# Performance work log

Measured on AMD Instinct MI355X. Metric: run time of the kernel, lower is better.

Reference implementation:

```python
import jax, jax.numpy as jnp
import numpy as np

N, H, W, PD, HID, NH = 2, 64, 64, 16, 128, 4
EPS = 1e-5


def _bn(x, g, b):
    # training-mode BatchNorm over (N, H, W) with biased variance, channels last
    m = jnp.mean(x, axis=(0, 1, 2), keepdims=True)
    v = jnp.var(x, axis=(0, 1, 2), keepdims=True)
    return (x - m) * jax.lax.rsqrt(v + EPS) * g + b


def _mha(x, in_w, in_b, out_w, out_b, nh):
    # torch nn.MultiheadAttention (batch_first) with packed qkv in_proj
    B, S, E = x.shape
    hd = E // nh
    q, k, v = jnp.split(x @ in_w.T + in_b, 3, axis=-1)
    def heads(t):
        return t.reshape(B, S, nh, hd).transpose(0, 2, 1, 3)  # B,nh,S,hd
    q, k, v = heads(q), heads(k), heads(v)
    a = jax.nn.softmax(jnp.einsum('bnqd,bnkd->bnqk', q, k) / np.float32(np.sqrt(hd)), axis=-1)
    o = jnp.einsum('bnqk,bnkd->bnqd', a, v).transpose(0, 2, 1, 3).reshape(B, S, E)
    return o @ out_w.T + out_b


def setup_inputs():
    key = jax.random.key(0)
    ks = jax.random.split(key, 32)
    def r(i, shape, s=0.1):
        return jax.random.normal(ks[i], shape, dtype=jnp.float32) * s
    mask = (jnp.arange(W) % 2) == 0  # alternating columns kept, M = W//2
    return {
        'kspace': jax.random.normal(ks[0], (N, 2, H, W), dtype=jnp.float32),
        'mask': mask,
        'pre_conv_w': r(1, (PD, 2), 0.5), 'pre_conv_b': r(2, (PD,)),
        'pre_pe_H': r(3, (H, PD)), 'pre_pe_W': r(4, (W, PD)),
        'res_conv1_w': r(5, (PD, PD), 0.2), 'res_conv1_b': r(6, (PD,)),
        'res_bn1_g': 1.0 + r(7, (PD,)), 'res_bn1_b': r(8, (PD,)),
        'res_conv2_w': r(9, (PD, PD), 0.2), 'res_conv2_b': r(10, (PD,)),
        'res_bn2_g': 1.0 + r(11, (PD,)), 'res_bn2_b': r(12, (PD,)),
        'proj_w': r(13, (HID, PD), 0.2), 'proj_b': r(14, (HID,)),
        'enc_in_w': r(15, (3 * HID, HID), 0.08), 'enc_in_b': r(16, (3 * HID,)),
        'enc_out_w': r(17, (HID, HID), 0.08), 'enc_out_b': r(18, (HID,)),
        'dec_pe_H': r(19, (H, HID)), 'dec_pe_W': r(20, (W, HID)),
        'dec_in_w': r(21, (3 * HID, HID), 0.08), 'dec_in_b': r(22, (3 * HID,)),
        'dec_out_w': r(23, (HID, HID), 0.08), 'dec_out_b': r(24, (HID,)),
        'masked_token': r(25, (HID,), 1.0),
        'post_w': r(26, (2, HID), 0.1), 'post_b': r(27, (2,)),
    }


def reference(kspace, mask, pre_conv_w, pre_conv_b, pre_pe_H, pre_pe_W,
              res_conv1_w, res_conv1_b, res_bn1_g, res_bn1_b,
              res_conv2_w, res_conv2_b, res_bn2_g, res_bn2_b,
              proj_w, proj_b, enc_in_w, enc_in_b, enc_out_w, enc_out_b,
              dec_pe_H, dec_pe_W, dec_in_w, dec_in_b, dec_out_w, dec_out_b,
              masked_token, post_w, post_b):
    cols = np.nonzero(np.asarray(mask))[0]  # static sampled columns
    M = cols.shape[0]
    # gather valid columns; channels last: [N, H, M, 2]
    x = kspace.transpose(0, 2, 3, 1)[:, :, cols, :]
    h = x @ pre_conv_w.T + pre_conv_b  # 1x1 conv -> [N, H, M, PD]
    h = h + (pre_pe_H[:, None, :] + pre_pe_W[cols][None, :, :])
    # PixelwiseConstantChannelResNet (1 layer)
    r1 = jax.nn.relu(_bn(h @ res_conv1_w.T + res_conv1_b, res_bn1_g, res_bn1_b))
    r2 = jax.nn.relu(_bn(r1 @ res_conv2_w.T + res_conv2_b, res_bn2_g, res_bn2_b))
    h = jax.nn.relu(h + r2)
    h = h @ proj_w.T + proj_b  # [N, H, M, HID]
    enc = _mha(h.reshape(N, H * M, HID), enc_in_w, enc_in_b, enc_out_w, enc_out_b, NH)
    # scatter: fill unmasked positions with masked_token, masked with encoder output
    dec = jnp.broadcast_to(masked_token, (N, H, W, HID))
    dec = dec.at[:, :, cols, :].set(enc.reshape(N, H, M, HID))
    dec = dec + (dec_pe_H[:, None, :] + dec_pe_W[None, :, :])
    dec = _mha(dec.reshape(N, H * W, HID), dec_in_w, dec_in_b, dec_out_w, dec_out_b, NH)
    out = dec.reshape(N, H, W, HID) @ post_w.T + post_b  # [N, H, W, 2]
    return out.transpose(0, 3, 1, 2)  # [N, 2, H, W]
```

## Files before the change

### kernel.cpp

```cpp
#include <hip/hip_runtime.h>
#include <math.h>

#define N_ 2
#define H_ 64
#define W_ 64
#define M_ 32
#define PD_ 16
#define HID_ 128
#define NH_ 4
#define HD_ 32
#define S_ENC 2048
#define S_DEC 4096
#define EPS_ 1e-5f
#define SCALE_ 0.17677669529663687f
#define SCALE2_ (0.17677669529663687f * 1.4426950408889634f)

#define OFF_H     0
#define OFF_T1    65536
#define OFF_T2    131072
#define OFF_STAT  196608
#define OFF_WP    196672
#define OFF_BP    202816
#define OFF_QBF   203264
#define OFF_KBF   727552
#define OFF_VTBF  1251840
#define OFF_ATTBF 1776128
#define OFF_XBF2  2300416
#define OFF_WBF   2824704

#define WOFF_ENC_OUT 0
#define WOFF_DEC_IN  16384
#define WOFF_DEC_OUT 65536

#define IB_MF   2048
#define IB_WC   320
#define IB_WP   24
#define IB_BP   2
#define IB_TOT  (IB_MF + IB_WC + IB_WP + IB_BP + 1)

typedef short bf16x8 __attribute__((ext_vector_type(8)));
typedef short bf16x4 __attribute__((ext_vector_type(4)));
typedef float f32x4 __attribute__((ext_vector_type(4)));

__device__ __forceinline__ short f2bf(float f) {
  union { float f; unsigned u; } v; v.f = f;
  unsigned r = v.u + 0x7FFFu + ((v.u >> 16) & 1u);
  return (short)(r >> 16);
}

__global__ void k_init(const float* __restrict__ eow, const float* __restrict__ dw,
                       const float* __restrict__ dow, const float* __restrict__ mt,
                       const float* __restrict__ peH, const float* __restrict__ peW,
                       const float* __restrict__ ew, const float* __restrict__ pw,
                       const float* __restrict__ pb, const float* __restrict__ eib,
                       short* __restrict__ wbf, short* __restrict__ xdec,
                       float* __restrict__ wp, float* __restrict__ bp,
                       float* __restrict__ stat) {
  int blk = blockIdx.x, tid = threadIdx.x;
  if (blk < IB_MF) {
    int idx = blk * 256 + tid;
    int j = idx & 127;
    int widx = (idx >> 7) & 31;
    int hh = (idx >> 12) & 63;
    int b = idx >> 18;
    int w = 2 * widx + 1;
    xdec[((size_t)(b * 4096 + hh * 64 + w)) * 128 + j] =
        f2bf(mt[j] + peH[hh * 128 + j] + peW[w * 128 + j]);
  } else if (blk < IB_MF + IB_WC) {
    int idx = (blk - IB_MF) * 256 + tid;
    float v;
    if (idx < 16384) v = eow[idx];
    else if (idx < 65536) v = dw[idx - 16384];
    else v = dow[idx - 65536];
    wbf[idx] = f2bf(v);
  } else if (blk < IB_MF + IB_WC + IB_WP) {
    int e = (blk - IB_MF - IB_WC) * 256 + tid;
    int row = e >> 4, k = e & 15;
    float a = 0.f;
    for (int j = 0; j < 128; j++) a = fmaf(ew[row * 128 + j], pw[j * 16 + k], a);
    wp[e] = a;
  } else if (blk < IB_MF + IB_WC + IB_WP + IB_BP) {
    int row = (blk - IB_MF - IB_WC - IB_WP) * 256 + tid;
    if (row < 384) {
      float a = eib[row];
      for (int j = 0; j < 128; j++) a = fmaf(ew[row * 128 + j], pb[j], a);
      bp[row] = a;
    }
  } else {
    if (tid < 64) stat[tid] = 0.f;
  }
}

__global__ void k_prelin_stats(const float* __restrict__ ks, const float* __restrict__ pcw,
                               const float* __restrict__ pcb, const float* __restrict__ peH,
                               const float* __restrict__ peW, const float* __restrict__ w1,
                               const float* __restrict__ b1, float* __restrict__ h,
                               float* __restrict__ t1, float* __restrict__ stat) {
  int tid = threadIdx.x;
  int pos = blockIdx.x * 256 + tid;
  int m = pos & 31, hh = (pos >> 5) & 63, b = pos >> 11;
  int w = 2 * m;
  float x0 = ks[((b * 2 + 0) * H_ + hh) * W_ + w];
  float x1 = ks[((b * 2 + 1) * H_ + hh) * W_ + w];
  float hv[16], tv[16];
#pragma unroll
  for (int c = 0; c < 16; c++)
    hv[c] = x0 * pcw[c * 2] + x1 * pcw[c * 2 + 1] + pcb[c]
            + peH[hh * PD_ + c] + peW[w * PD_ + c];
#pragma unroll
  for (int c = 0; c < 16; c += 4)
    *(float4*)&h[pos * 16 + c] = make_float4(hv[c], hv[c + 1], hv[c + 2], hv[c + 3]);
#pragma unroll
  for (int c = 0; c < 16; c++) {
    float a = b1[c];
#pragma unroll
    for (int k = 0; k < 16; k++) a = fmaf(hv[k], w1[c * 16 + k], a);
    tv[c] = a;
    t1[pos * 16 + c] = a;
  }
  __shared__ float tl[256][17];
#pragma unroll
  for (int c = 0; c < 16; c++) tl[tid][c] = tv[c];
  __syncthreads();
  int c = tid & 15, g = tid >> 4;
  float s = 0.f, s2 = 0.f;
#pragma unroll
  for (int r = 0; r < 16; r++) {
    float v = tl[g * 16 + r][c];
    s += v; s2 += v * v;
  }
  __shared__ float ps[16][16], ps2[16][16];
  ps[g][c] = s; ps2[g][c] = s2;
  __syncthreads();
  if (tid < 16) {
    float S = 0.f, S2 = 0.f;
#pragma unroll
    for (int g2 = 0; g2 < 16; g2++) { S += ps[g2][tid]; S2 += ps2[g2][tid]; }
    atomicAdd(&stat[tid], S);
    atomicAdd(&stat[16 + tid], S2);
  }
}

__global__ void k_bnlin_stats(const float* __restrict__ t1, const float* __restrict__ stat,
                              const float* __restrict__ g1, const float* __restrict__ bb1,
                              const float* __restrict__ w2, const float* __restrict__ b2,
                              float* __restrict__ t2, float* __restrict__ statw) {
  int tid = threadIdx.x;
  int pos = blockIdx.x * 256 + tid;
  const float inv = 1.f / 4096.f;
  float r[16];
#pragma unroll
  for (int k = 0; k < 16; k++) {
    float mu = stat[k] * inv;
    float var = stat[16 + k] * inv - mu * mu;
    float v = (t1[pos * 16 + k] - mu) * rsqrtf(var + EPS_) * g1[k] + bb1[k];
    r[k] = fmaxf(v, 0.f);
  }
  float tv[16];
#pragma unroll
  for (int c = 0; c < 16; c++) {
    float a = b2[c];
#pragma unroll
    for (int k = 0; k < 16; k++) a = fmaf(r[k], w2[c * 16 + k], a);
    tv[c] = a;
    t2[pos * 16 + c] = a;
  }
  __shared__ float tl[256][17];
#pragma unroll
  for (int c = 0; c < 16; c++) tl[tid][c] = tv[c];
  __syncthreads();
  int c = tid & 15, g = tid >> 4;
  float s = 0.f, s2 = 0.f;
#pragma unroll
  for (int rr = 0; rr < 16; rr++) {
    float v = tl[g * 16 + rr][c];
    s += v; s2 += v * v;
  }
  __shared__ float ps[16][16], ps2[16][16];
  ps[g][c] = s; ps2[g][c] = s2;
  __syncthreads();
  if (tid < 16) {
    float S = 0.f, S2 = 0.f;
#pragma unroll
    for (int g2 = 0; g2 < 16; g2++) { S += ps[g2][tid]; S2 += ps2[g2][tid]; }
    atomicAdd(&statw[32 + tid], S);
    atomicAdd(&statw[48 + tid], S2);
  }
}

__global__ __launch_bounds__(256)
void k_fqkv_enc(const float* __restrict__ h, const float* __restrict__ t2,
                const float* __restrict__ stat, const float* __restrict__ g2,
                const float* __restrict__ bb2, const float* __restrict__ wp,
                const float* __restrict__ bp, short* __restrict__ qbf,
                short* __restrict__ kbf, short* __restrict__ vtbf) {
  int tid = threadIdx.x;
  int p0 = blockIdx.x * 32;
  __shared__ float hf[32][20];
  const float inv = 1.f / 4096.f;
#pragma unroll
  for (int i = 0; i < 2; i++) {
    int idx = tid * 2 + i;
    int lp = idx >> 4, c = idx & 15;
    int pos = p0 + lp;
    float mu = stat[32 + c] * inv;
    float var = stat[48 + c] * inv - mu * mu;
    float v = (t2[pos * 16 + c] - mu) * rsqrtf(var + EPS_) * g2[c] + bb2[c];
    v = fmaxf(v, 0.f);
    hf[lp][c] = fmaxf(h[pos * 16 + c] + v, 0.f);
  }
  __syncthreads();
  int bb = p0 >> 11;
  int sbase = p0 & 2047;
  {
    int col = tid;
    float wc[16];
#pragma unroll
    for (int k = 0; k < 16; k += 4) *(float4*)&wc[k] = *(const float4*)&wp[col * 16 + k];
    float bpv = bp[col];
    int isQ = (col < 128);
    int c2 = isQ ? col : (col - 128);
    int hd = c2 >> 5, d = c2 & 31;
    short* dst = isQ ? qbf : kbf;
    float sc = isQ ? SCALE2_ : 1.f;
    size_t rowb = ((size_t)(bb * 4 + hd) * S_ENC + sbase) * 32 + d;
    for (int lp = 0; lp < 32; lp++) {
      float a = bpv;
#pragma unroll
      for (int k = 0; k < 16; k++) a = fmaf(hf[lp][k], wc[k], a);
      dst[rowb + (size_t)lp * 32] = f2bf(a * sc);
    }
  }
  if (tid < 128) {
    int col = 256 + tid;
    float wc[16];
#pragma unroll
    for (int k = 0; k < 16; k += 4) *(float4*)&wc[k] = *(const float4*)&wp[col * 16 + k];
    float bpv = bp[col];
    int c2 = tid;
    int hd = c2 >> 5, d = c2 & 31;
    size_t rowb = ((size_t)(bb * 4 + hd) * 32 + d) * S_ENC + sbase;
    for (int lp4 = 0; lp4 < 32; lp4 += 4) {
      bf16x4 pk;
#pragma unroll
      for (int r = 0; r < 4; r++) {
        float a = bpv;
#pragma unroll
        for (int k = 0; k < 16; k++) a = fmaf(hf[lp4 + r][k], wc[k], a);
        pk[r] = f2bf(a);
      }
      *(bf16x4*)&vtbf[rowb + lp4] = pk;
    }
  }
}

#define MGEMM_STAGE_AND_FRAGS                                                   \
  __shared__ short As[64 * 128];                                                \
  __shared__ short Wl[64 * 128];                                                \
  int tid = threadIdx.x;                                                        \
  _Pragma("unroll")                                                             \
  for (int i = 0; i < 4; i++) {                                                 \
    int idx = i * 256 + tid;                                                    \
    int row = idx >> 4, c = idx & 15, slot = c ^ (row & 7);                     \
    *(bf16x8*)&As[row * 128 + slot * 8] =                                       \
        *(const bf16x8*)&abf[(size_t)(rb + row) * 128 + c * 8];                 \
    *(bf16x8*)&Wl[row * 128 + slot * 8] =                                       \
        *(const bf16x8*)&wbf[(size_t)(ob + row) * 128 + c * 8];                 \
  }                                                                             \
  __syncthreads();                                                              \
  int lane = tid & 63, wv = tid >> 6;                                           \
  int l15 = lane & 15, quad = lane >> 4;                                        \
  int m0 = wv * 16;                                                             \
  f32x4 acc[4];                                                                 \
  acc[0] = acc[1] = acc[2] = acc[3] = (f32x4){0.f, 0.f, 0.f, 0.f};              \
  _Pragma("unroll")                                                             \
  for (int kk = 0; kk < 4; kk++) {                                              \
    int sl = ((kk * 4 + quad) ^ (l15 & 7)) * 8;                                 \
    bf16x8 af = *(const bf16x8*)&As[(m0 + l15) * 128 + sl];                     \
    _Pragma("unroll")                                                           \
    for (int nt = 0; nt < 4; nt++) {                                            \
      bf16x8 wf = *(const bf16x8*)&Wl[(nt * 16 + l15) * 128 + sl];              \
      acc[nt] = __builtin_amdgcn_mfma_f32_16x16x32_bf16(af, wf, acc[nt], 0, 0, 0); \
    }                                                                           \
  }

__global__ __launch_bounds__(256)
void k_mgemm_qkv_dec(const short* __restrict__ abf, const short* __restrict__ wbf,
                     const float* __restrict__ bias, short* __restrict__ qbf,
                     short* __restrict__ kbf, short* __restrict__ vtbf) {
  const int S = 4096;
  int rb = blockIdx.x * 64, ob = blockIdx.y * 64;
  MGEMM_STAGE_AND_FRAGS
#pragma unroll
  for (int nt = 0; nt < 4; nt++) {
    int col = ob + nt * 16 + l15;
    float bv = bias[col];
    if (ob < 128) {
      int hd = col >> 5, d = col & 31;
#pragma unroll
      for (int r = 0; r < 4; r++) {
        int grow = rb + m0 + quad * 4 + r;
        int bb = grow >> 12, s = grow & (S - 1);
        qbf[((size_t)(bb * 4 + hd) * S + s) * 32 + d] =
            f2bf((acc[nt][r] + bv) * SCALE2_);
      }
    } else if (ob < 256) {
      int c2 = col - 128, hd = c2 >> 5, d = c2 & 31;
#pragma unroll
      for (int r = 0; r < 4; r++) {
        int grow = rb + m0 + quad * 4 + r;
        int bb = grow >> 12, s = grow & (S - 1);
        kbf[((size_t)(bb * 4 + hd) * S + s) * 32 + d] = f2bf(acc[nt][r] + bv);
      }
    } else {
      int c2 = col - 256, hd = c2 >> 5, d = c2 & 31;
      int grow0 = rb + m0 + quad * 4;
      int bb = grow0 >> 12, s0 = grow0 & (S - 1);
      bf16x4 pk;
#pragma unroll
      for (int r = 0; r < 4; r++) pk[r] = f2bf(acc[nt][r] + bv);
      *(bf16x4*)&vtbf[((size_t)(bb * 4 + hd) * 32 + d) * S + s0] = pk;
    }
  }
}

__global__ __launch_bounds__(256)
void k_mgemm_out_enc(const short* __restrict__ abf, const short* __restrict__ wbf,
                     const float* __restrict__ bias, const float* __restrict__ peH,
                     const float* __restrict__ peW, short* __restrict__ xdec) {
  int rb = blockIdx.x * 64, ob = blockIdx.y * 64;
  MGEMM_STAGE_AND_FRAGS
#pragma unroll
  for (int nt = 0; nt < 4; nt++) {
    int col = ob + nt * 16 + l15;
    float bv = bias[col];
#pragma unroll
    for (int r = 0; r < 4; r++) {
      int grow = rb + m0 + quad * 4 + r;
      int bb = grow >> 11, rem = grow & 2047;
      int hhh = rem >> 5, m = rem & 31, w = 2 * m;
      xdec[((size_t)(bb * 4096 + hhh * 64 + w)) * 128 + col] =
          f2bf(acc[nt][r] + bv + peH[hhh * 128 + col] + peW[w * 128 + col]);
    }
  }
}

__global__ __launch_bounds__(256)
void k_mgemm_out_post(const short* __restrict__ abf, const short* __restrict__ wbf,
                      const float* __restrict__ bias, const float* __restrict__ pw,
                      const float* __restrict__ pb, float* __restrict__ outp) {
  int rb = blockIdx.x * 64;
  __shared__ short As[64 * 128];
  __shared__ short Wl[128 * 128];
  int tid = threadIdx.x;
#pragma unroll
  for (int i = 0; i < 4; i++) {
    int idx = i * 256 + tid;
    int row = idx >> 4, c = idx & 15, slot = c ^ (row & 7);
    *(bf16x8*)&As[row * 128 + slot * 8] =
        *(const bf16x8*)&abf[(size_t)(rb + row) * 128 + c * 8];
  }
#pragma unroll
  for (int i = 0; i < 8; i++) {
    int idx = i * 256 + tid;
    int row = idx >> 4, c = idx & 15, slot = c ^ (row & 7);
    *(bf16x8*)&Wl[row * 128 + slot * 8] =
        *(const bf16x8*)&wbf[(size_t)row * 128 + c * 8];
  }
  __syncthreads();
  int lane = tid & 63, wv = tid >> 6;
  int l15 = lane & 15, quad = lane >> 4;
  int m0 = wv * 16;
  f32x4 acc[8];
#pragma unroll
  for (int nt = 0; nt < 8; nt++) acc[nt] = (f32x4){0.f, 0.f, 0.f, 0.f};
#pragma unroll
  for (int kk = 0; kk < 4; kk++) {
    int sl = ((kk * 4 + quad) ^ (l15 & 7)) * 8;
    bf16x8 af = *(const bf16x8*)&As[(m0 + l15) * 128 + sl];
#pragma unroll
    for (int nt = 0; nt < 8; nt++) {
      bf16x8 wf = *(const bf16x8*)&Wl[(nt * 16 + l15) * 128 + sl];
      acc[nt] = __builtin_amdgcn_mfma_f32_16x16x32_bf16(af, wf, acc[nt], 0, 0, 0);
    }
  }
  float bv[8], pw0[8], pw1[8];
#pragma unroll
  for (int nt = 0; nt < 8; nt++) {
    int col = nt * 16 + l15;
    bv[nt] = bias[col];
    pw0[nt] = pw[col];
    pw1[nt] = pw[128 + col];
  }
  float pb0 = pb[0], pb1 = pb[1];
#pragma unroll
  for (int r = 0; r < 4; r++) {
    float pc0 = 0.f, pc1 = 0.f;
#pragma unroll
    for (int nt = 0; nt < 8; nt++) {
      float yv = acc[nt][r] + bv[nt];
      pc0 = fmaf(yv, pw0[nt], pc0);
      pc1 = fmaf(yv, pw1[nt], pc1);
    }
    pc0 += __shfl_xor(pc0, 1); pc0 += __shfl_xor(pc0, 2);
    pc0 += __shfl_xor(pc0, 4); pc0 += __shfl_xor(pc0, 8);
    pc1 += __shfl_xor(pc1, 1); pc1 += __shfl_xor(pc1, 2);
    pc1 += __shfl_xor(pc1, 4); pc1 += __shfl_xor(pc1, 8);
    if (l15 == 0) {
      int grow = rb + m0 + quad * 4 + r;
      int bb = grow >> 12, hw = grow & 4095;
      outp[(size_t)(bb * 2 + 0) * 4096 + hw] = pc0 + pb0;
      outp[(size_t)(bb * 2 + 1) * 4096 + hw] = pc1 + pb1;
    }
  }
}

template <int S>
__global__ __launch_bounds__(1024)
__attribute__((amdgpu_waves_per_eu(8)))
void k_attn11(const short* __restrict__ qbf, const short* __restrict__ kbf,
              const short* __restrict__ vtbf, short* __restrict__ outb) {
  __shared__ __align__(16) char smem[65536];
  short* kb4 = (short*)smem;
  short* vt4 = (short*)(smem + 16384);
  short* pb4 = (short*)(smem + 32768);
  float* abuf = (float*)smem;
  float* lb   = (float*)(smem + 24576);

  int qt = blockIdx.x, hh = blockIdx.y, b = blockIdx.z;
  int tid = threadIdx.x;
  int lane = tid & 63;
  int wv = tid >> 6;
  int qtr = wv >> 2;
  int wv4 = wv & 3;
  int l15 = lane & 15, quad = lane >> 4;
  int t256 = tid & 255;

  int bh = b * NH_ + hh;
  const short* kg = kbf + (size_t)bh * S * 32;
  const short* vg = vtbf + (size_t)bh * 32 * S;
  short* kbh = kb4 + qtr * 2048;
  short* vth = vt4 + qtr * 2048;

  bf16x8 qf = *(const bf16x8*)&qbf[((size_t)bh * S + qt * 64 + wv4 * 16 + l15) * 32
                                   + quad * 8];

  f32x4 acc[2];
  acc[0] = (f32x4){0.f, 0.f, 0.f, 0.f};
  acc[1] = (f32x4){0.f, 0.f, 0.f, 0.f};
  float lpart = 0.f;

  int srowK = t256 >> 2, schK = t256 & 3;
  int slotK = schK ^ ((srowK >> 1) & 3);
  int srowV = t256 >> 3, sslV = t256 & 7;
  int sgV = sslV ^ (srowV & 7);

  short* prow = pb4 + (size_t)(qtr * 64 + wv4 * 16 + l15) * 64;
  int kq0 = qtr * (S / 4);
  int kxor = (l15 >> 1) & 3;
  int pxor = l15 & 7;

  const short* kgp = kg + (size_t)(kq0 + srowK) * 32 + schK * 8;
  const short* vgp = vg + (size_t)srowV * S + kq0 + sgV * 8;
  short* kdst = kbh + srowK * 32 + slotK * 8;
  short* vdst = vth + srowV * 64 + sslV * 8;

  bf16x8 krg = *(const bf16x8*)kgp;
  bf16x8 vrg = *(const bf16x8*)vgp;

  constexpr int NIT = S / 256;
  for (int it = 0; it < NIT; ++it) {
    asm volatile("s_waitcnt lgkmcnt(0)" ::: "memory");
    __builtin_amdgcn_s_barrier();
    asm volatile("" ::: "memory");
    *(bf16x8*)kdst = krg;
    *(bf16x8*)vdst = vrg;
    if (it + 1 < NIT) {
      kgp += 64 * 32;
      vgp += 64;
      krg = *(const bf16x8*)kgp;
      vrg = *(const bf16x8*)vgp;
    }
    asm volatile("s_waitcnt lgkmcnt(0)" ::: "memory");
    __builtin_amdgcn_s_barrier();
    asm volatile("" ::: "memory");

    f32x4 s[4];
#pragma unroll
    for (int t = 0; t < 4; t++) {
      bf16x8 kf = *(const bf16x8*)&kbh[(t * 16 + l15) * 32 + ((quad ^ kxor) * 8)];
      s[t] = __builtin_amdgcn_mfma_f32_16x16x32_bf16(
          kf, qf, (f32x4){0.f, 0.f, 0.f, 0.f}, 0, 0, 0);
    }

#pragma unroll
    for (int t = 0; t < 4; t++) {
      float p0 = __builtin_exp2f(s[t][0]);
      float p1 = __builtin_exp2f(s[t][1]);
      float p2 = __builtin_exp2f(s[t][2]);
      float p3 = __builtin_exp2f(s[t][3]);
      lpart += (p0 + p1) + (p2 + p3);
      unsigned w0, w1;
      asm("v_cvt_pk_bf16_f32 %0, %1, %2" : "=v"(w0) : "v"(p0), "v"(p1));
      asm("v_cvt_pk_bf16_f32 %0, %1, %2" : "=v"(w1) : "v"(p2), "v"(p3));
      uint2 pk;
      pk.x = w0;
      pk.y = w1;
      int cc = t * 2 + (quad >> 1);
      *(uint2*)&prow[(cc ^ pxor) * 8 + (quad & 1) * 4] = pk;
    }

#pragma unroll
    for (int kh = 0; kh < 2; kh++) {
      int cc2 = kh * 4 + quad;
      bf16x8 pf = *(const bf16x8*)&prow[(cc2 ^ pxor) * 8];
#pragma unroll
      for (int nt = 0; nt < 2; nt++) {
        bf16x8 vf = *(const bf16x8*)&vth[(nt * 16 + l15) * 64 + ((cc2 ^ pxor) * 8)];
        acc[nt] = __builtin_amdgcn_mfma_f32_16x16x32_bf16(vf, pf, acc[nt], 0, 0, 0);
      }
    }
  }

  lpart += __shfl_xor(lpart, 16);
  lpart += __shfl_xor(lpart, 32);

  __syncthreads();
  if (qtr > 0) {
#pragma unroll
    for (int nt = 0; nt < 2; nt++)
#pragma unroll
      for (int r = 0; r < 4; r++)
        abuf[(qtr - 1) * 2048 + wv4 * 512 + (nt * 16 + quad * 4 + r) * 16 + l15] =
            acc[nt][r];
    if (quad == 0) lb[(qtr - 1) * 64 + wv4 * 16 + l15] = lpart;
  }
  __syncthreads();
  if (qtr == 0) {
    int li = wv4 * 16 + l15;
    float ltot = lpart + lb[li] + lb[64 + li] + lb[128 + li];
    float inv = 1.f / ltot;
    int base = wv4 * 512;
    short* op = outb + ((size_t)(b * S + qt * 64 + wv4 * 16 + l15)) * 128 + hh * 32;
#pragma unroll
    for (int nt = 0; nt < 2; nt++) {
      bf16x4 pk;
#pragma unroll
      for (int r = 0; r < 4; r++) {
        int d = nt * 16 + quad * 4 + r;
        float v = acc[nt][r] + abuf[base + d * 16 + l15]
                + abuf[2048 + base + d * 16 + l15]
                + abuf[4096 + base + d * 16 + l15];
        pk[r] = f2bf(v * inv);
      }
      *(bf16x4*)&op[nt * 16 + quad * 4] = pk;
    }
  }
}

extern "C" void kernel_launch(void* const* d_in, const int* in_sizes, int n_in,
                              void* d_out, int out_size, void* d_ws, size_t ws_size,
                              hipStream_t stream) {
  const float* ks        = (const float*)d_in[0];
  const float* pre_conv_w = (const float*)d_in[2];
  const float* pre_conv_b = (const float*)d_in[3];
  const float* pre_pe_H   = (const float*)d_in[4];
  const float* pre_pe_W   = (const float*)d_in[5];
  const float* w1  = (const float*)d_in[6];
  const float* b1  = (const float*)d_in[7];
  const float* g1  = (const float*)d_in[8];
  const float* bb1 = (const float*)d_in[9];
  const float* w2  = (const float*)d_in[10];
  const float* b2  = (const float*)d_in[11];
  const float* g2  = (const float*)d_in[12];
  const float* bb2 = (const float*)d_in[13];
  const float* proj_w = (const float*)d_in[14];
  const float* proj_b = (const float*)d_in[15];
  const float* enc_in_w  = (const float*)d_in[16];
  const float* enc_in_b  = (const float*)d_in[17];
  const float* enc_out_w = (const float*)d_in[18];
  const float* enc_out_b = (const float*)d_in[19];
  const float* dec_pe_H  = (const float*)d_in[20];
  const float* dec_pe_W  = (const float*)d_in[21];
  const float* dec_in_w  = (const float*)d_in[22];
  const float* dec_in_b  = (const float*)d_in[23];
  const float* dec_out_w = (const float*)d_in[24];
  const float* dec_out_b = (const float*)d_in[25];
  const float* masked_token = (const float*)d_in[26];
  const float* post_w = (const float*)d_in[27];
  const float* post_b = (const float*)d_in[28];
  float* out = (float*)d_out;

  float* ws    = (float*)d_ws;
  float* h     = ws + OFF_H;
  float* t1    = ws + OFF_T1;
  float* t2    = ws + OFF_T2;
  float* stat  = ws + OFF_STAT;
  float* wp    = ws + OFF_WP;
  float* bp    = ws + OFF_BP;
  short* qbf   = (short*)(ws + OFF_QBF);
  short* kbfb  = (short*)(ws + OFF_KBF);
  short* vtbfb = (short*)(ws + OFF_VTBF);
  short* attbf = (short*)(ws + OFF_ATTBF);
  short* xbf2  = (short*)(ws + OFF_XBF2);
  short* wbf   = (short*)(ws + OFF_WBF);

  k_init<<<IB_TOT, 256, 0, stream>>>(enc_out_w, dec_in_w, dec_out_w, masked_token,
                                     dec_pe_H, dec_pe_W, enc_in_w, proj_w, proj_b,
                                     enc_in_b, wbf, xbf2, wp, bp, stat);
  k_prelin_stats<<<16, 256, 0, stream>>>(ks, pre_conv_w, pre_conv_b, pre_pe_H,
                                         pre_pe_W, w1, b1, h, t1, stat);
  k_bnlin_stats<<<16, 256, 0, stream>>>(t1, stat, g1, bb1, w2, b2, t2, stat);
  k_fqkv_enc<<<128, 256, 0, stream>>>(h, t2, stat, g2, bb2, wp, bp,
                                      qbf, kbfb, vtbfb);
  k_attn11<S_ENC><<<dim3(S_ENC / 64, NH_, N_), 1024, 0, stream>>>(qbf, kbfb, vtbfb, attbf);
  k_mgemm_out_enc<<<dim3(S_ENC * N_ / 64, 2), 256, 0, stream>>>(
      attbf, wbf + WOFF_ENC_OUT, enc_out_b, dec_pe_H, dec_pe_W, xbf2);
  k_mgemm_qkv_dec<<<dim3(S_DEC * N_ / 64, 6), 256, 0, stream>>>(
      xbf2, wbf + WOFF_DEC_IN, dec_in_b, qbf, kbfb, vtbfb);
  k_attn11<S_DEC><<<dim3(S_DEC / 64, NH_, N_), 1024, 0, stream>>>(qbf, kbfb, vtbfb, attbf);
  k_mgemm_out_post<<<S_DEC * N_ / 64, 256, 0, stream>>>(
      attbf, wbf + WOFF_DEC_OUT, dec_out_b, post_w, post_b, out);
}
```

Measured before the change: 210.4 us.

## Keep P in registers via permuted V load and double-buffer K/V tiles

The attention kernel no longer writes the exponentiated scores to LDS and reads them back. Instead it packs them straight into the MFMA B operand in registers, and changes how V is gathered from global memory (two 4-element loads at permuted offsets) so the key ordering matches the register layout. K and V tiles are double-buffered in shared memory, which removes one of the two barriers per iteration. This cuts LDS traffic and synchronisation, at the cost of narrower global loads for V and more live registers.

```diff
diff --git a/kernel.cpp b/kernel.cpp
--- a/kernel.cpp
+++ b/kernel.cpp
@@ -422,8 +422,7 @@
               const short* __restrict__ vtbf, short* __restrict__ outb) {
   __shared__ __align__(16) char smem[65536];
   short* kb4 = (short*)smem;
-  short* vt4 = (short*)(smem + 16384);
-  short* pb4 = (short*)(smem + 32768);
+  short* vt4 = (short*)(smem + 32768);
   float* abuf = (float*)smem;
   float* lb   = (float*)(smem + 24576);
 
@@ -454,70 +453,76 @@
   int slotK = schK ^ ((srowK >> 1) & 3);
   int srowV = t256 >> 3, sslV = t256 & 7;
   int sgV = sslV ^ (srowV & 7);
-
-  short* prow = pb4 + (size_t)(qtr * 64 + wv4 * 16 + l15) * 64;
+  int gbV = ((sgV >> 2) << 5) + ((sgV & 3) << 2);
+
   int kq0 = qtr * (S / 4);
   int kxor = (l15 >> 1) & 3;
-  int pxor = l15 & 7;
+  int vsl = l15 & 7;
 
   const short* kgp = kg + (size_t)(kq0 + srowK) * 32 + schK * 8;
-  const short* vgp = vg + (size_t)srowV * S + kq0 + sgV * 8;
+  const short* vgp0 = vg + (size_t)srowV * S + kq0 + gbV;
+  const short* vgp1 = vgp0 + 16;
   short* kdst = kbh + srowK * 32 + slotK * 8;
   short* vdst = vth + srowV * 64 + sslV * 8;
 
   bf16x8 krg = *(const bf16x8*)kgp;
-  bf16x8 vrg = *(const bf16x8*)vgp;
+  bf16x4 vr0 = *(const bf16x4*)vgp0;
+  bf16x4 vr1 = *(const bf16x4*)vgp1;
 
   constexpr int NIT = S / 256;
   for (int it = 0; it < NIT; ++it) {
+    int co = (it & 1) << 13;
+    *(bf16x8*)(kdst + co) = krg;
+    *(bf16x8*)(vdst + co) = __builtin_shufflevector(vr0, vr1, 0, 1, 2, 3, 4, 5, 6, 7);
+    if (it + 1 < NIT) {
+      kgp += 64 * 32;
+      vgp0 += 64;
+      vgp1 += 64;
+      krg = *(const bf16x8*)kgp;
+      vr0 = *(const bf16x4*)vgp0;
+      vr1 = *(const bf16x4*)vgp1;
+    }
     asm volatile("s_waitcnt lgkmcnt(0)" ::: "memory");
     __builtin_amdgcn_s_barrier();
     asm volatile("" ::: "memory");
-    *(bf16x8*)kdst = krg;
-    *(bf16x8*)vdst = vrg;
-    if (it + 1 < NIT) {
-      kgp += 64 * 32;
-      vgp += 64;
-      krg = *(const bf16x8*)kgp;
-      vrg = *(const bf16x8*)vgp;
-    }
-    asm volatile("s_waitcnt lgkmcnt(0)" ::: "memory");
-    __builtin_amdgcn_s_barrier();
-    asm volatile("" ::: "memory");
+
+    const short* kbhc = kbh + co;
+    const short* vthc = vth + co;
 
     f32x4 s[4];
 #pragma unroll
     for (int t = 0; t < 4; t++) {
-      bf16x8 kf = *(const bf16x8*)&kbh[(t * 16 + l15) * 32 + ((quad ^ kxor) * 8)];
+      bf16x8 kf = *(const bf16x8*)&kbhc[(t * 16 + l15) * 32 + ((quad ^ kxor) * 8)];
       s[t] = __builtin_amdgcn_mfma_f32_16x16x32_bf16(
           kf, qf, (f32x4){0.f, 0.f, 0.f, 0.f}, 0, 0, 0);
     }
 
+    float pe[4][4];
 #pragma unroll
     for (int t = 0; t < 4; t++) {
-      float p0 = __builtin_exp2f(s[t][0]);
-      float p1 = __builtin_exp2f(s[t][1]);
-      float p2 = __builtin_exp2f(s[t][2]);
-      float p3 = __builtin_exp2f(s[t][3]);
-      lpart += (p0 + p1) + (p2 + p3);
-      unsigned w0, w1;
-      asm("v_cvt_pk_bf16_f32 %0, %1, %2" : "=v"(w0) : "v"(p0), "v"(p1));
-      asm("v_cvt_pk_bf16_f32 %0, %1, %2" : "=v"(w1) : "v"(p2), "v"(p3));
-      uint2 pk;
-      pk.x = w0;
-      pk.y = w1;
-      int cc = t * 2 + (quad >> 1);
-      *(uint2*)&prow[(cc ^ pxor) * 8 + (quad & 1) * 4] = pk;
+      pe[t][0] = __builtin_exp2f(s[t][0]);
+      pe[t][1] = __builtin_exp2f(s[t][1]);
+      pe[t][2] = __builtin_exp2f(s[t][2]);
+      pe[t][3] = __builtin_exp2f(s[t][3]);
+      lpart += (pe[t][0] + pe[t][1]) + (pe[t][2] + pe[t][3]);
     }
 
 #pragma unroll
     for (int kh = 0; kh < 2; kh++) {
-      int cc2 = kh * 4 + quad;
-      bf16x8 pf = *(const bf16x8*)&prow[(cc2 ^ pxor) * 8];
+      union { unsigned u[4]; bf16x8 v; } pf;
+      asm("v_cvt_pk_bf16_f32 %0, %1, %2"
+          : "=v"(pf.u[0]) : "v"(pe[2 * kh][0]), "v"(pe[2 * kh][1]));
+      asm("v_cvt_pk_bf16_f32 %0, %1, %2"
+          : "=v"(pf.u[1]) : "v"(pe[2 * kh][2]), "v"(pe[2 * kh][3]));
+      asm("v_cvt_pk_bf16_f32 %0, %1, %2"
+          : "=v"(pf.u[2]) : "v"(pe[2 * kh + 1][0]), "v"(pe[2 * kh + 1][1]));
+      asm("v_cvt_pk_bf16_f32 %0, %1, %2"
+          : "=v"(pf.u[3]) : "v"(pe[2 * kh + 1][2]), "v"(pe[2 * kh + 1][3]));
 #pragma unroll
       for (int nt = 0; nt < 2; nt++) {
-        bf16x8 vf = *(const bf16x8*)&vth[(nt * 16 + l15) * 64 + ((cc2 ^ pxor) * 8)];
-        acc[nt] = __builtin_amdgcn_mfma_f32_16x16x32_bf16(vf, pf, acc[nt], 0, 0, 0);
+        bf16x8 vf = *(const bf16x8*)&vthc[(nt * 16 + l15) * 64
+                                          + (((kh * 4 + quad) ^ vsl) * 8)];
+        acc[nt] = __builtin_amdgcn_mfma_f32_16x16x32_bf16(vf, pf.v, acc[nt], 0, 0, 0);
       }
     }
   }
```

After: 203.7 us. -3.2%, faster.
